# Kernel tuning notes

Hardware: AMD Instinct MI355X
Metric: run time of the kernel (lower is better)

The kernel has to match this reference:

```python
import jax, jax.numpy as jnp
import numpy as np

MAX_STEPS = 12          # ns = ceil((t1-t0)/0.2) <= ceil(2/0.2) = 10 for unit dirs, unit sphere
BASE_STEP = 0.2
ABSORPTION = 0.1
SCATTERING = 0.1
DENSITY = 6.0
SIGMA = SCATTERING + ABSORPTION + 0.4   # 0.6, used in sample_transparency
BG = jnp.array([0.572, 0.772, 0.921], dtype=jnp.float32)
LIGHT_COLOR = jnp.array([1.3, 0.3, 0.9], dtype=jnp.float32)
RO = jnp.array([0.0, 0.0, 3.0], dtype=jnp.float32)   # hard-coded ray origin in original


def setup_inputs() -> dict:
    key = jax.random.key(0)
    W = H = 1024
    u = jnp.linspace(-0.5, 0.5, W, dtype=jnp.float32)
    v = jnp.linspace(-0.5, 0.5, H, dtype=jnp.float32)
    uu, vv = jnp.meshgrid(u, v, indexing='ij')
    d = jnp.stack([uu, vv, -jnp.ones_like(uu)], axis=-1)          # camera at z=3 looking at origin
    d = d + 0.001 * jax.random.normal(key, d.shape, dtype=jnp.float32)  # randn jitter
    dirs = d / jnp.linalg.norm(d, axis=-1, keepdims=True)          # unit directions -> bounded ns
    scene = jnp.array([[0.0, 0.0, 0.0, 1.0]], dtype=jnp.float32)   # unit sphere at origin
    return {"scene": scene, "dirs": dirs}


def _ray_march(scene, dirs):
    center = scene[0, 0:3]
    radius = scene[0, 3]
    rd = dirs                                      # [W,H,3]
    oc = RO - center                               # [3]
    a = jnp.sum(rd * rd, axis=-1)                  # [W,H]
    b = 2.0 * jnp.sum(rd * oc, axis=-1)
    c = jnp.dot(oc, oc) - radius * radius
    disc = b * b - 4.0 * a * c
    sq = jnp.sqrt(jnp.where(disc > 0, disc, 1.0))  # safe sqrt (masked later)
    x1 = (-b - sq) / (2.0 * a)
    x2 = (-b + sq) / (2.0 * a)
    # flag: disc>=0 and not (x1<0 and x2<0); since x1<=x2 this is x2>=0
    hit = (disc >= 0) & (x2 >= 0)                  # [W,H]
    t0 = jnp.maximum(x1, 0.0)                      # inside -> t0 = 0
    t1 = x2
    seg = t1 - t0
    ns = jnp.ceil(seg / BASE_STEP)                 # [W,H] float step count
    ns_safe = jnp.maximum(ns, 1.0)
    step = seg / ns_safe                           # per-pixel step size
    s = jnp.exp(-SIGMA * step)                     # per-step sample_transparency

    # static march over MAX_STEPS, masked by i < ns
    steps = jnp.arange(MAX_STEPS, dtype=jnp.float32)                 # [K]
    smask = (steps[None, None, :] < ns[..., None]) & hit[..., None]  # [W,H,K]
    t = t1[..., None] - (steps + 0.5) * step[..., None]              # [W,H,K]
    p = RO + t[..., None] * rd[..., None, :]                         # [W,H,K,3] sample points
    pc = p - center
    # light ray: origin p, direction (0,1,0) -> a=1
    lb = 2.0 * pc[..., 1]
    lc = jnp.sum(pc * pc, axis=-1) - radius * radius
    ld = lb * lb - 4.0 * lc
    lsq = jnp.sqrt(jnp.where(ld > 0, ld, 1.0))
    vt1 = (-lb + lsq) / 2.0
    lhit = (ld >= 0) & (vt1 >= 0)
    la = jnp.exp(-DENSITY * (SCATTERING + ABSORPTION) * vt1)         # light attenuation
    acc = jnp.sum(jnp.where(smask & lhit, la, 0.0), axis=-1)         # [W,H]

    # closed form of the original loop:
    #   result = sum_i la_i * light_color * s^(i+1) * scat*dens*step * s^(ns-i)
    #          = light_color * scat*dens*step * s^(ns+1) * sum_i la_i
    transparency = s ** ns
    result = (SCATTERING * DENSITY) * step * (s ** (ns + 1.0)) * acc  # [W,H]
    color_hit = BG * transparency[..., None] + LIGHT_COLOR * result[..., None]
    pixels = jnp.where(hit[..., None], color_hit, BG)                 # [W,H,3]
    return pixels


def reference(scene, dirs):
    return _ray_march(scene, dirs)
```

## Files before the change

### kernel.cpp

```cpp
#include <hip/hip_runtime.h>
#include <math.h>

__device__ __forceinline__ float fmulr(float a, float b) { return __fmul_rn(a, b); }
__device__ __forceinline__ float faddr(float a, float b) { return __fadd_rn(a, b); }
__device__ __forceinline__ float fsubr(float a, float b) { return __fsub_rn(a, b); }

struct Col { float x, y, z; };

__device__ __forceinline__ Col shade(float rdx, float rdy, float rdz,
                                     float cx, float cy, float cz,
                                     float rr,
                                     float ocx, float ocy, float ocz,
                                     float cc)
{
    const float BGx = 0.572f, BGy = 0.772f, BGz = 0.921f;
    Col out = {BGx, BGy, BGz};

    float a = faddr(faddr(fmulr(rdx, rdx), fmulr(rdy, rdy)), fmulr(rdz, rdz));
    float b = fmulr(2.0f, faddr(faddr(fmulr(rdx, ocx), fmulr(rdy, ocy)), fmulr(rdz, ocz)));
    float disc = fsubr(fmulr(b, b), fmulr(fmulr(4.0f, a), cc));
    if (disc < 0.0f) return out;

    float sq = sqrtf(disc > 0.0f ? disc : 1.0f);
    float twoa = fmulr(2.0f, a);
    float x2 = faddr(-b, sq) / twoa;
    if (x2 < 0.0f) return out;
    float x1 = fsubr(-b, sq) / twoa;

    float t0 = fmaxf(x1, 0.0f);
    float t1 = x2;
    float seg = fsubr(t1, t0);
    float ns = ceilf(seg / 0.2f);
    float ns_safe = fmaxf(ns, 1.0f);
    float step = seg / ns_safe;
    int nsi = (int)fminf(ns, 12.0f);

    float acc = 0.0f;
    for (int k = 0; k < nsi; ++k) {
        float kph = (float)k + 0.5f;
        float t = fsubr(t1, fmulr(kph, step));
        float pcx = fsubr(faddr(0.0f, fmulr(t, rdx)), cx);
        float pcy = fsubr(faddr(0.0f, fmulr(t, rdy)), cy);
        float pcz = fsubr(faddr(3.0f, fmulr(t, rdz)), cz);
        float lb = fmulr(2.0f, pcy);
        float lc = fsubr(faddr(faddr(fmulr(pcx, pcx), fmulr(pcy, pcy)), fmulr(pcz, pcz)), rr);
        float ld = fsubr(fmulr(lb, lb), fmulr(4.0f, lc));
        if (ld >= 0.0f) {
            float lsq = sqrtf(ld > 0.0f ? ld : 1.0f);
            float vt1 = fmulr(faddr(-lb, lsq), 0.5f);
            if (vt1 >= 0.0f) {
                acc += __expf(-1.2f * vt1);
            }
        }
    }

    float sn  = __expf(-0.6f * (step * ns));
    float sn1 = __expf(-0.6f * (step * (ns + 1.0f)));
    float result = 0.6f * step * sn1 * acc;
    out.x = BGx * sn + 1.3f * result;
    out.y = BGy * sn + 0.3f * result;
    out.z = BGz * sn + 0.9f * result;
    return out;
}

__global__ __launch_bounds__(256)
void raymarch_kernel(const float* __restrict__ scene,
                     const float4* __restrict__ dirs4,
                     float4* __restrict__ out4,
                     int npix)
{
    int tid = blockIdx.x * blockDim.x + threadIdx.x;
    int base = tid * 4;
    if (base >= npix) return;

    float cx = scene[0], cy = scene[1], cz = scene[2], r = scene[3];
    float rr = fmulr(r, r);
    float ocx = fsubr(0.0f, cx);
    float ocy = fsubr(0.0f, cy);
    float ocz = fsubr(3.0f, cz);
    float cc = fsubr(faddr(faddr(fmulr(ocx, ocx), fmulr(ocy, ocy)), fmulr(ocz, ocz)), rr);

    if (base + 3 < npix) {
        float4 v0 = dirs4[tid * 3 + 0];
        float4 v1 = dirs4[tid * 3 + 1];
        float4 v2 = dirs4[tid * 3 + 2];

        Col c0 = shade(v0.x, v0.y, v0.z, cx, cy, cz, rr, ocx, ocy, ocz, cc);
        Col c1 = shade(v0.w, v1.x, v1.y, cx, cy, cz, rr, ocx, ocy, ocz, cc);
        Col c2 = shade(v1.z, v1.w, v2.x, cx, cy, cz, rr, ocx, ocy, ocz, cc);
        Col c3 = shade(v2.y, v2.z, v2.w, cx, cy, cz, rr, ocx, ocy, ocz, cc);

        out4[tid * 3 + 0] = make_float4(c0.x, c0.y, c0.z, c1.x);
        out4[tid * 3 + 1] = make_float4(c1.y, c1.z, c2.x, c2.y);
        out4[tid * 3 + 2] = make_float4(c2.z, c3.x, c3.y, c3.z);
    } else {
        const float* dirs = (const float*)dirs4;
        float* out = (float*)out4;
        for (int p = base; p < npix; ++p) {
            Col c = shade(dirs[3 * p + 0], dirs[3 * p + 1], dirs[3 * p + 2],
                          cx, cy, cz, rr, ocx, ocy, ocz, cc);
            out[3 * p + 0] = c.x;
            out[3 * p + 1] = c.y;
            out[3 * p + 2] = c.z;
        }
    }
}

extern "C" void kernel_launch(void* const* d_in, const int* in_sizes, int n_in,
                              void* d_out, int out_size, void* d_ws, size_t ws_size,
                              hipStream_t stream) {
    const float* scene = (const float*)d_in[0];
    const float* dirs  = (const float*)d_in[1];
    float* out = (float*)d_out;

    int npix = in_sizes[1] / 3;
    int nthreads = (npix + 3) / 4;
    dim3 block(256);
    dim3 grid((nthreads + 255) / 256);
    raymarch_kernel<<<grid, block, 0, stream>>>(scene, (const float4*)dirs,
                                                (float4*)out, npix);
}
```

Measured before the change: 75.87 us.

## Use one pixel per thread and add unit-sphere fast path

Changes the mapping from four pixels per thread with float4 loads and stores to one pixel per thread with scalar strided loads and stores. It also adds a specialised shading path, picked at runtime, for a unit sphere at the origin, which drops the center subtractions and constant setup. The finer mapping gives more threads to hide the divergent march loop, at the cost of wider-vector memory accesses. The fast path is guarded by a runtime check, so the general path stays correct.

```diff
diff --git a/kernel.cpp b/kernel.cpp
--- a/kernel.cpp
+++ b/kernel.cpp
@@ -7,11 +7,58 @@
 
 struct Col { float x, y, z; };
 
-__device__ __forceinline__ Col shade(float rdx, float rdy, float rdz,
-                                     float cx, float cy, float cz,
-                                     float rr,
-                                     float ocx, float ocy, float ocz,
-                                     float cc)
+__device__ __forceinline__ Col shade1(float rdx, float rdy, float rdz)
+{
+    const float BGx = 0.572f, BGy = 0.772f, BGz = 0.921f;
+    Col out = {BGx, BGy, BGz};
+
+    float a = faddr(faddr(fmulr(rdx, rdx), fmulr(rdy, rdy)), fmulr(rdz, rdz));
+    float b = fmulr(2.0f, fmulr(rdz, 3.0f));
+    float disc = fsubr(fmulr(b, b), fmulr(fmulr(4.0f, a), 8.0f));
+    if (disc < 0.0f) return out;
+
+    float sq = sqrtf(disc > 0.0f ? disc : 1.0f);
+    float twoa = fmulr(2.0f, a);
+    float x2 = faddr(-b, sq) / twoa;
+    if (x2 < 0.0f) return out;
+    float x1 = fsubr(-b, sq) / twoa;
+
+    float t0 = fmaxf(x1, 0.0f);
+    float t1 = x2;
+    float seg = fsubr(t1, t0);
+    float ns = ceilf(seg / 0.2f);
+    float step = seg / fmaxf(ns, 1.0f);
+    int nsi = (int)fminf(ns, 12.0f);
+
+    float acc = 0.0f;
+    for (int k = 0; k < nsi; ++k) {
+        float t = fsubr(t1, fmulr((float)k + 0.5f, step));
+        float pcx = fmulr(t, rdx);
+        float pcy = fmulr(t, rdy);
+        float pcz = faddr(3.0f, fmulr(t, rdz));
+        float lb = fmulr(2.0f, pcy);
+        float lc = fsubr(faddr(faddr(fmulr(pcx, pcx), fmulr(pcy, pcy)), fmulr(pcz, pcz)), 1.0f);
+        float ld = fsubr(fmulr(lb, lb), fmulr(4.0f, lc));
+        if (ld >= 0.0f) {
+            float lsq = sqrtf(ld > 0.0f ? ld : 1.0f);
+            float vt1 = fmulr(faddr(-lb, lsq), 0.5f);
+            if (vt1 >= 0.0f) acc += __expf(-1.2f * vt1);
+        }
+    }
+
+    float sn  = __expf(-0.6f * (step * ns));
+    float sn1 = __expf(-0.6f * (step * (ns + 1.0f)));
+    float result = 0.6f * step * sn1 * acc;
+    out.x = BGx * sn + 1.3f * result;
+    out.y = BGy * sn + 0.3f * result;
+    out.z = BGz * sn + 0.9f * result;
+    return out;
+}
+
+__device__ __forceinline__ Col shadeg(float rdx, float rdy, float rdz,
+                                      float cx, float cy, float cz,
+                                      float rr, float ocx, float ocy, float ocz,
+                                      float cc)
 {
     const float BGx = 0.572f, BGy = 0.772f, BGz = 0.921f;
     Col out = {BGx, BGy, BGz};
@@ -31,14 +78,12 @@
     float t1 = x2;
     float seg = fsubr(t1, t0);
     float ns = ceilf(seg / 0.2f);
-    float ns_safe = fmaxf(ns, 1.0f);
-    float step = seg / ns_safe;
+    float step = seg / fmaxf(ns, 1.0f);
     int nsi = (int)fminf(ns, 12.0f);
 
     float acc = 0.0f;
     for (int k = 0; k < nsi; ++k) {
-        float kph = (float)k + 0.5f;
-        float t = fsubr(t1, fmulr(kph, step));
+        float t = fsubr(t1, fmulr((float)k + 0.5f, step));
         float pcx = fsubr(faddr(0.0f, fmulr(t, rdx)), cx);
         float pcy = fsubr(faddr(0.0f, fmulr(t, rdy)), cy);
         float pcz = fsubr(faddr(3.0f, fmulr(t, rdz)), cz);
@@ -48,9 +93,7 @@
         if (ld >= 0.0f) {
             float lsq = sqrtf(ld > 0.0f ? ld : 1.0f);
             float vt1 = fmulr(faddr(-lb, lsq), 0.5f);
-            if (vt1 >= 0.0f) {
-                acc += __expf(-1.2f * vt1);
-            }
+            if (vt1 >= 0.0f) acc += __expf(-1.2f * vt1);
         }
     }
 
@@ -65,45 +108,34 @@
 
 __global__ __launch_bounds__(256)
 void raymarch_kernel(const float* __restrict__ scene,
-                     const float4* __restrict__ dirs4,
-                     float4* __restrict__ out4,
+                     const float* __restrict__ dirs,
+                     float* __restrict__ out,
                      int npix)
 {
-    int tid = blockIdx.x * blockDim.x + threadIdx.x;
-    int base = tid * 4;
-    if (base >= npix) return;
+    int p = blockIdx.x * blockDim.x + threadIdx.x;
+    if (p >= npix) return;
+
+    float rdx = dirs[3 * p + 0];
+    float rdy = dirs[3 * p + 1];
+    float rdz = dirs[3 * p + 2];
 
     float cx = scene[0], cy = scene[1], cz = scene[2], r = scene[3];
-    float rr = fmulr(r, r);
-    float ocx = fsubr(0.0f, cx);
-    float ocy = fsubr(0.0f, cy);
-    float ocz = fsubr(3.0f, cz);
-    float cc = fsubr(faddr(faddr(fmulr(ocx, ocx), fmulr(ocy, ocy)), fmulr(ocz, ocz)), rr);
 
-    if (base + 3 < npix) {
-        float4 v0 = dirs4[tid * 3 + 0];
-        float4 v1 = dirs4[tid * 3 + 1];
-        float4 v2 = dirs4[tid * 3 + 2];
+    Col c;
+    if (cx == 0.0f && cy == 0.0f && cz == 0.0f && r == 1.0f) {
+        c = shade1(rdx, rdy, rdz);
+    } else {
+        float rr = fmulr(r, r);
+        float ocx = fsubr(0.0f, cx);
+        float ocy = fsubr(0.0f, cy);
+        float ocz = fsubr(3.0f, cz);
+        float cc = fsubr(faddr(faddr(fmulr(ocx, ocx), fmulr(ocy, ocy)), fmulr(ocz, ocz)), rr);
+        c = shadeg(rdx, rdy, rdz, cx, cy, cz, rr, ocx, ocy, ocz, cc);
+    }
 
-        Col c0 = shade(v0.x, v0.y, v0.z, cx, cy, cz, rr, ocx, ocy, ocz, cc);
-        Col c1 = shade(v0.w, v1.x, v1.y, cx, cy, cz, rr, ocx, ocy, ocz, cc);
-        Col c2 = shade(v1.z, v1.w, v2.x, cx, cy, cz, rr, ocx, ocy, ocz, cc);
-        Col c3 = shade(v2.y, v2.z, v2.w, cx, cy, cz, rr, ocx, ocy, ocz, cc);
-
-        out4[tid * 3 + 0] = make_float4(c0.x, c0.y, c0.z, c1.x);
-        out4[tid * 3 + 1] = make_float4(c1.y, c1.z, c2.x, c2.y);
-        out4[tid * 3 + 2] = make_float4(c2.z, c3.x, c3.y, c3.z);
-    } else {
-        const float* dirs = (const float*)dirs4;
-        float* out = (float*)out4;
-        for (int p = base; p < npix; ++p) {
-            Col c = shade(dirs[3 * p + 0], dirs[3 * p + 1], dirs[3 * p + 2],
-                          cx, cy, cz, rr, ocx, ocy, ocz, cc);
-            out[3 * p + 0] = c.x;
-            out[3 * p + 1] = c.y;
-            out[3 * p + 2] = c.z;
-        }
-    }
+    out[3 * p + 0] = c.x;
+    out[3 * p + 1] = c.y;
+    out[3 * p + 2] = c.z;
 }
 
 extern "C" void kernel_launch(void* const* d_in, const int* in_sizes, int n_in,
@@ -114,9 +146,7 @@
     float* out = (float*)d_out;
 
     int npix = in_sizes[1] / 3;
-    int nthreads = (npix + 3) / 4;
     dim3 block(256);
-    dim3 grid((nthreads + 255) / 256);
-    raymarch_kernel<<<grid, block, 0, stream>>>(scene, (const float4*)dirs,
-                                                (float4*)out, npix);
+    dim3 grid((npix + 255) / 256);
+    raymarch_kernel<<<grid, block, 0, stream>>>(scene, dirs, out, npix);
 }
```

Result: faster. 71.94 us (-5.2%).
